# Performance work log

Measured on AMD Instinct MI355X. Metric: run time of the kernel, lower is better.

Reference implementation:

```python
import jax, jax.numpy as jnp
import numpy as np

TOP_K = 2
CAPACITY_FACTOR = 1.0


def setup_inputs() -> dict:
    key = jax.random.key(0)
    ks = jax.random.split(key, 4)
    S, M, E, V = 32768, 512, 64, 2048
    return {
        "x": jax.random.normal(ks[0], (S, M), jnp.float32),
        "wg": jax.random.normal(ks[1], (E, M), jnp.float32) * (1.0 / np.sqrt(M)),
        "fc1_w": jax.random.normal(ks[2], (E, M, V), jnp.float32) * (1.0 / np.sqrt(M)),
        "fc1_b": jnp.zeros((E, V), jnp.float32),
        "fc2_w": jax.random.normal(ks[3], (E, V, M), jnp.float32) * (1.0 / np.sqrt(V)),
        "fc2_b": jnp.zeros((E, M), jnp.float32),
    }


def _moe_forward(x, wg, fc1_w, fc1_b, fc2_w, fc2_b):
    S, M = x.shape
    E = wg.shape[0]
    K = TOP_K
    # capacity = top_k * int(cap_factor * ceil(S / E))  (static, from shapes)
    C = K * int(CAPACITY_FACTOR * ((S + E - 1) // E))

    # --- gating ---
    logits = x @ wg.T                                    # [S, E]
    gates = jax.nn.softmax(logits, axis=-1)              # [S, E]
    topk_idx = jax.lax.top_k(logits, K)[1]               # [S, K] int32
    masks = jax.nn.one_hot(topk_idx, E, dtype=logits.dtype)  # [S, K, E]
    gates_s = jnp.einsum('se,ske->sk', gates, masks)     # [S, K]

    # load-balance aux loss (fp32 path of load_balance)
    me = gates.sum(axis=0)                               # [E]
    ce = masks[:, 0, :].sum(axis=0)                      # [E]
    l_loss = jnp.sum(me * ce) * (E / (S * S))

    # --- cumsum capacity locations with per-k offsets (acc_base) ---
    counts = masks.sum(axis=0)                           # [K, E]
    prev_counts = jnp.concatenate(
        [jnp.zeros((1, E), logits.dtype), jnp.cumsum(counts, axis=0)[:-1]], axis=0)
    cums = jnp.cumsum(masks, axis=0) - 1.0               # fast_cumsum_sub_one per k
    locs = jnp.einsum('ske,ske->sk', cums + prev_counts[None], masks).astype(jnp.int32)

    # normalize top-k gates (top_k > 1 branch)
    denom = jnp.maximum(gates_s.sum(axis=1, keepdims=True),
                        jnp.finfo(gates_s.dtype).eps)
    gates_n = gates_s / denom                            # [S, K]

    # --- encode: scatter tokens into [E, C, M], overflow tokens dropped ---
    valid = locs < C                                     # [S, K]
    flat_pos = jnp.where(valid, topk_idx.astype(jnp.int32) * C + locs, E * C)
    src = jnp.broadcast_to(x[:, None, :], (S, K, M)).reshape(-1, M)
    disp = jnp.zeros((E * C + 1, M), x.dtype).at[flat_pos.reshape(-1)].add(src)
    disp = disp[:E * C].reshape(E, C, M)                 # world_size=1: AllToAll = id

    # --- fused FFN experts: relu(x @ fc1 + b1) @ fc2 + b2 ---
    h = jax.nn.relu(jnp.einsum('ecm,emv->ecv', disp, fc1_w) + fc1_b[:, None, :])
    eout = jnp.einsum('ecv,evm->ecm', h, fc2_w) + fc2_b[:, None, :]

    # --- decode/combine: gather expert slots, weight by normalized gates ---
    eflat = jnp.concatenate([eout.reshape(E * C, M),
                             jnp.zeros((1, M), eout.dtype)], axis=0)
    gathered = eflat[flat_pos]                           # [S, K, M]
    y = jnp.einsum('sk,skm->sm', gates_n * valid.astype(gates_n.dtype), gathered)
    return y, l_loss


def reference(x, wg, fc1_w, fc1_b, fc2_w, fc2_b):
    return _moe_forward(x, wg, fc1_w, fc1_b, fc2_w, fc2_b)
```

## Files before the change

### kernel.cpp

```cpp
#include <hip/hip_runtime.h>
#include <hip/hip_bf16.h>
#include <stdint.h>

#define S_TOK 32768
#define M_DIM 512
#define E_NUM 64
#define V_DIM 2048
#define CAP   1024

typedef __attribute__((ext_vector_type(8))) short short8;
typedef __attribute__((ext_vector_type(4))) float f32x4;

__device__ __forceinline__ unsigned short f2bf(float f) {
  unsigned int u = __float_as_uint(f);
  unsigned int r = (u + 0x7fffu + ((u >> 16) & 1u)) >> 16;
  return (unsigned short)r;
}
__device__ __forceinline__ float bf2f(unsigned short h) {
  return __uint_as_float(((unsigned int)h) << 16);
}

__device__ __forceinline__ void gload16(const void* g, void* lds) {
  __builtin_amdgcn_global_load_lds(
      (const __attribute__((address_space(1))) void*)g,
      (__attribute__((address_space(3))) void*)lds, 16, 0, 0);
}

#define GATE_BLKS (S_TOK / 16)
#define TR_BLKS   16384

struct PrepSmem {
  union {
    float ts[128][65];
    struct {
      float4 xs4[16 * 128];
      float mered[4][64];
      int cered[4][64];
    } g;
  };
};

__global__ __launch_bounds__(256) void prep_kernel(
    const float* __restrict__ x, const float* __restrict__ wg,
    int* __restrict__ topk, float* __restrict__ gates_n,
    float* __restrict__ me_part, int* __restrict__ ce_part,
    unsigned short* __restrict__ xbf,
    const float* __restrict__ w1, unsigned short* __restrict__ o1,
    const float* __restrict__ w2, unsigned short* __restrict__ o2) {
  __shared__ PrepSmem sm;
  int tid = threadIdx.x;

  if (blockIdx.x >= GATE_BLKS) {
    int t = blockIdx.x - GATE_BLKS;
    int which = t >> 13;
    t &= 8191;
    int R = which ? V_DIM : M_DIM;
    int Cc = which ? M_DIM : V_DIM;
    int nbx = Cc / 64;
    int b = t >> 7;
    int tt = t & 127;
    const float* ip = (which ? w2 : w1) + (size_t)b * R * Cc;
    unsigned short* op = (which ? o2 : o1) + (size_t)b * R * Cc;
    int c0 = (tt % nbx) * 64, r0 = (tt / nbx) * 128;
    #pragma unroll
    for (int i = 0; i < 8; ++i) {
      int chunk = i * 256 + tid;
      int row = chunk >> 4;
      int c4 = (chunk & 15) * 4;
      float4 v = *reinterpret_cast<const float4*>(&ip[(size_t)(r0 + row) * Cc + c0 + c4]);
      sm.ts[row][c4 + 0] = v.x; sm.ts[row][c4 + 1] = v.y;
      sm.ts[row][c4 + 2] = v.z; sm.ts[row][c4 + 3] = v.w;
    }
    __syncthreads();
    #pragma unroll
    for (int i = 0; i < 4; ++i) {
      int chunk = i * 256 + tid;
      int c = chunk >> 4;
      int m8 = (chunk & 15) * 8;
      short8 o;
      #pragma unroll
      for (int j = 0; j < 8; ++j) o[j] = (short)f2bf(sm.ts[m8 + j][c]);
      *reinterpret_cast<short8*>(&op[(size_t)(c0 + c) * R + r0 + m8]) = o;
    }
    return;
  }

  int l = tid & 63, w = tid >> 6;
  int tb = blockIdx.x * 16;
  const float4* xg4 = reinterpret_cast<const float4*>(x) + (size_t)tb * 128;
  ushort4* xb4 = reinterpret_cast<ushort4*>(xbf) + (size_t)tb * 128;
  #pragma unroll
  for (int i = 0; i < 8; ++i) {
    float4 v = xg4[i * 256 + tid];
    sm.g.xs4[i * 256 + tid] = v;
    ushort4 o;
    o.x = f2bf(v.x); o.y = f2bf(v.y); o.z = f2bf(v.z); o.w = f2bf(v.w);
    xb4[i * 256 + tid] = o;
  }
  __syncthreads();

  const float4* wg4 = reinterpret_cast<const float4*>(wg) + (size_t)l * 128;
  float acc[4] = {0.f, 0.f, 0.f, 0.f};
  for (int i0 = 0; i0 < 128; i0 += 8) {
    float4 wv[8];
    #pragma unroll
    for (int u = 0; u < 8; ++u) wv[u] = wg4[i0 + u];
    #pragma unroll
    for (int u = 0; u < 8; ++u) {
      #pragma unroll
      for (int t = 0; t < 4; ++t) {
        float4 xv = sm.g.xs4[(w * 4 + t) * 128 + i0 + u];
        acc[t] += xv.x * wv[u].x; acc[t] += xv.y * wv[u].y;
        acc[t] += xv.z * wv[u].z; acc[t] += xv.w * wv[u].w;
      }
    }
  }

  float melocal = 0.f;
  int celocal = 0;
  for (int t = 0; t < 4; ++t) {
    float v = acc[t];
    float bv = v; int bi = l;
    #pragma unroll
    for (int off = 32; off; off >>= 1) {
      float ov = __shfl_xor(bv, off);
      int oi = __shfl_xor(bi, off);
      if (ov > bv || (ov == bv && oi < bi)) { bv = ov; bi = oi; }
    }
    float v2 = (l == bi) ? -INFINITY : v;
    float bv2 = v2; int bi2 = l;
    #pragma unroll
    for (int off = 32; off; off >>= 1) {
      float ov = __shfl_xor(bv2, off);
      int oi = __shfl_xor(bi2, off);
      if (ov > bv2 || (ov == bv2 && oi < bi2)) { bv2 = ov; bi2 = oi; }
    }
    float ex = expf(v - bv);
    float s = ex;
    #pragma unroll
    for (int off = 32; off; off >>= 1) s += __shfl_xor(s, off);
    melocal += ex / s;
    if (l == bi) celocal += 1;
    if (l == 0) {
      int sidx = tb + w * 4 + t;
      topk[sidx * 2 + 0] = bi;
      topk[sidx * 2 + 1] = bi2;
      float g1 = 1.0f / s;
      float g2 = expf(bv2 - bv) / s;
      float denom = fmaxf(g1 + g2, 1.1920929e-07f);
      gates_n[sidx * 2 + 0] = g1 / denom;
      gates_n[sidx * 2 + 1] = g2 / denom;
    }
  }
  sm.g.mered[w][l] = melocal;
  sm.g.cered[w][l] = celocal;
  __syncthreads();
  if (tid < 64) {
    me_part[blockIdx.x * 64 + tid] =
        sm.g.mered[0][tid] + sm.g.mered[1][tid] + sm.g.mered[2][tid] + sm.g.mered[3][tid];
    ce_part[blockIdx.x * 64 + tid] =
        sm.g.cered[0][tid] + sm.g.cered[1][tid] + sm.g.cered[2][tid] + sm.g.cered[3][tid];
  }
}

__global__ __launch_bounds__(256) void rank_kernel(const int* __restrict__ topk,
                                                   int* __restrict__ dest,
                                                   int* __restrict__ slot_map) {
  int e = blockIdx.x;
  int tid = threadIdx.x;
  int l = tid & 63, w = tid >> 6;
  int4 minus1 = {-1, -1, -1, -1};
  reinterpret_cast<int4*>(slot_map + e * CAP)[tid] = minus1;

  const int2* tk = reinterpret_cast<const int2*>(topk);
  int base = tid * 128;
  int c0 = 0, c1 = 0;
  for (int j = 0; j < 128; ++j) {
    int2 p = tk[base + j];
    c0 += (p.x == e); c1 += (p.y == e);
  }
  int i0 = c0, i1 = c1;
  #pragma unroll
  for (int off = 1; off < 64; off <<= 1) {
    int t0 = __shfl_up(i0, off);
    int t1 = __shfl_up(i1, off);
    if (l >= off) { i0 += t0; i1 += t1; }
  }
  __shared__ int ws0[4], ws1[4], wo0[4], wo1[4], tot0s;
  if (l == 63) { ws0[w] = i0; ws1[w] = i1; }
  __syncthreads();
  if (tid == 0) {
    int a = 0, b = 0;
    #pragma unroll
    for (int j = 0; j < 4; ++j) { wo0[j] = a; a += ws0[j]; wo1[j] = b; b += ws1[j]; }
    tot0s = a;
  }
  __syncthreads();
  int loc0 = wo0[w] + i0 - c0;
  int loc1 = tot0s + wo1[w] + i1 - c1;
  for (int j = 0; j < 128; ++j) {
    int s = base + j;
    int2 p = tk[s];
    if (p.x == e) {
      int d = (loc0 < CAP) ? e * CAP + loc0 : -1;
      dest[s * 2] = d;
      if (d >= 0) slot_map[d] = s;
      loc0++;
    }
    if (p.y == e) {
      int d = (loc1 < CAP) ? e * CAP + loc1 : -1;
      dest[s * 2 + 1] = d;
      if (d >= 0) slot_map[d] = s;
      loc1++;
    }
  }
}

#define PH_TOP                                                                 \
  __builtin_amdgcn_sched_barrier(0);                                           \
  __builtin_amdgcn_s_barrier();                                                \
  asm volatile("s_waitcnt lgkmcnt(0)" ::: "memory");                           \
  __builtin_amdgcn_sched_barrier(0);                                           \
  __builtin_amdgcn_s_setprio(1);
#define PH_BOT                                                                 \
  __builtin_amdgcn_s_setprio(0);                                               \
  __builtin_amdgcn_sched_barrier(0);                                           \
  __builtin_amdgcn_s_barrier();

struct SmemGemm {
  union {
    struct {
      unsigned short A[2][256 * 64];
      unsigned short B[2][256 * 64];
    } st;
    unsigned short C[256 * 258];
  };
};

template <int KD, int ND, int NBX, int NBY, bool GATHER, bool RELU>
__global__ __launch_bounds__(512, 2) void gemm8_kernel(
    const unsigned short* __restrict__ A,
    const unsigned short* __restrict__ BT,
    const float* __restrict__ bias,
    const int* __restrict__ slot_map,
    unsigned short* __restrict__ out) {
  constexpr int NT = KD / 64;
  __shared__ SmemGemm sm;

  const int tid = threadIdx.x;
  const int l = tid & 63;
  const int w = tid >> 6;
  const int wm = w >> 2;
  const int wn = w & 3;
  const int lr = l & 15;
  const int lk8 = l >> 4;

  const int nwg = E_NUM * NBX * NBY;
  const int cpx = nwg >> 3;
  int lid = ((int)blockIdx.x % 8) * cpx + (int)blockIdx.x / 8;
  const int e = lid / (NBX * NBY);
  int rem = lid % (NBX * NBY);
  const int n0 = (rem / NBY) * 256;
  const int r0 = (rem % NBY) * 256;

  const int cg8 = (((l & 7) ^ (l >> 3)) * 8);

  uint32_t offA[2][2], offB[2][2], ldsA[2][2], ldsB[2][2];
  #pragma unroll
  for (int sel = 0; sel < 2; ++sel) {
    #pragma unroll
    for (int i = 0; i < 2; ++i) {
      int lr128 = i * 64 + w * 8 + (l >> 3);
      int ar = ((lr128 >> 6) * 128) + sel * 64 + (lr128 & 63);
      int br = ((lr128 >> 5) * 64) + sel * 32 + (lr128 & 31);
      ldsA[sel][i] = ar * 64 + (l & 7) * 8;
      ldsB[sel][i] = br * 64 + (l & 7) * 8;
      int arow;
      if (GATHER) {
        int s = slot_map[e * CAP + r0 + ar];
        if (s < 0) s = 0;
        arow = s;
      } else {
        arow = e * CAP + r0 + ar;
      }
      offA[sel][i] = (uint32_t)arow * KD + cg8;
      offB[sel][i] = (uint32_t)(n0 + br) * KD + cg8;
    }
  }
  const unsigned short* Bexp = BT + (size_t)e * ND * KD;

  const int sg0 = ((0 + lk8) ^ (lr & 7)) * 8;
  const int sg1 = ((4 + lk8) ^ (lr & 7)) * 8;

#define STAGE_A(sel, p, kt)                                                    \
  do {                                                                         \
    gload16(A + offA[sel][0] + (kt) * 64, &sm.st.A[p][ldsA[sel][0]]);          \
    gload16(A + offA[sel][1] + (kt) * 64, &sm.st.A[p][ldsA[sel][1]]);          \
  } while (0)
#define STAGE_B(sel, p, kt)                                                    \
  do {                                                                         \
    gload16(Bexp + offB[sel][0] + (kt) * 64, &sm.st.B[p][ldsB[sel][0]]);       \
    gload16(Bexp + offB[sel][1] + (kt) * 64, &sm.st.B[p][ldsB[sel][1]]);       \
  } while (0)
#define RD_A(p, mh, mi, ks)                                                    \
  (*reinterpret_cast<const short8*>(                                           \
      &sm.st.A[p][(wm * 128 + (mh) * 64 + (mi) * 16 + lr) * 64 + ((ks) ? sg1 : sg0)]))
#define RD_B(p, nh, ni, ks)                                                    \
  (*reinterpret_cast<const short8*>(                                           \
      &sm.st.B[p][(wn * 64 + (nh) * 32 + (ni) * 16 + lr) * 64 + ((ks) ? sg1 : sg0)]))

  short8 afr[2][4][2];
  short8 bfr[2][2];
  f32x4 acc[8][4];
  f32x4 zero = {0.f, 0.f, 0.f, 0.f};
  #pragma unroll
  for (int m = 0; m < 8; ++m)
    #pragma unroll
    for (int n = 0; n < 4; ++n) acc[m][n] = zero;

  STAGE_A(0, 0, 0); STAGE_A(1, 0, 0); STAGE_B(0, 0, 0); STAGE_B(1, 0, 0);
  STAGE_A(0, 1, 1); STAGE_A(1, 1, 1); STAGE_B(0, 1, 1);
  asm volatile("s_waitcnt vmcnt(6)" ::: "memory");
  __builtin_amdgcn_sched_barrier(0);
  __builtin_amdgcn_s_barrier();

#define GROUP(k, p)                                                            \
  {                                                                            \
               \
    _Pragma("unroll") for (int mi = 0; mi < 4; ++mi) {                         \
      afr[0][mi][0] = RD_A(p, 0, mi, 0);                                       \
      afr[0][mi][1] = RD_A(p, 0, mi, 1);                                       \
    }                                                                          \
    _Pragma("unroll") for (int ni = 0; ni < 2; ++ni) {                         \
      bfr[ni][0] = RD_B(p, 0, ni, 0);                                          \
      bfr[ni][1] = RD_B(p, 0, ni, 1);                                          \
    }                                                                          \
    if ((k) + 1 < NT) { STAGE_B(1, (p) ^ 1, (k) + 1); }                        \
    PH_TOP                                                                     \
    _Pragma("unroll") for (int mi = 0; mi < 4; ++mi)                           \
      _Pragma("unroll") for (int ni = 0; ni < 2; ++ni) {                       \
        acc[mi][ni] = __builtin_amdgcn_mfma_f32_16x16x32_bf16(                 \
            afr[0][mi][0], bfr[ni][0], acc[mi][ni], 0, 0, 0);                  \
        acc[mi][ni] = __builtin_amdgcn_mfma_f32_16x16x32_bf16(                 \
            afr[0][mi][1], bfr[ni][1], acc[mi][ni], 0, 0, 0);                  \
      }                                                                        \
    PH_BOT                                                                     \
                 \
    _Pragma("unroll") for (int mi = 0; mi < 4; ++mi) {                         \
      afr[1][mi][0] = RD_A(p, 1, mi, 0);                                       \
      afr[1][mi][1] = RD_A(p, 1, mi, 1);                                       \
    }                                                                          \
    if ((k) + 2 < NT) { STAGE_A(0, p, (k) + 2); }                              \
    PH_TOP                                                                     \
    _Pragma("unroll") for (int mi = 0; mi < 4; ++mi)                           \
      _Pragma("unroll") for (int ni = 0; ni < 2; ++ni) {                       \
        acc[4 + mi][ni] = __builtin_amdgcn_mfma_f32_16x16x32_bf16(             \
            afr[1][mi][0], bfr[ni][0], acc[4 + mi][ni], 0, 0, 0);              \
        acc[4 + mi][ni] = __builtin_amdgcn_mfma_f32_16x16x32_bf16(             \
            afr[1][mi][1], bfr[ni][1], acc[4 + mi][ni], 0, 0, 0);              \
      }                                                                        \
    PH_BOT                                                                     \
                 \
    _Pragma("unroll") for (int ni = 0; ni < 2; ++ni) {                         \
      bfr[ni][0] = RD_B(p, 1, ni, 0);                                          \
      bfr[ni][1] = RD_B(p, 1, ni, 1);                                          \
    }                                                                          \
    if ((k) + 2 < NT) { STAGE_A(1, p, (k) + 2); }                              \
    PH_TOP                                                                     \
    _Pragma("unroll") for (int mi = 0; mi < 4; ++mi)                           \
      _Pragma("unroll") for (int ni = 0; ni < 2; ++ni) {                       \
        acc[mi][2 + ni] = __builtin_amdgcn_mfma_f32_16x16x32_bf16(             \
            afr[0][mi][0], bfr[ni][0], acc[mi][2 + ni], 0, 0, 0);              \
        acc[mi][2 + ni] = __builtin_amdgcn_mfma_f32_16x16x32_bf16(             \
            afr[0][mi][1], bfr[ni][1], acc[mi][2 + ni], 0, 0, 0);              \
      }                                                                        \
    PH_BOT                                                                     \
             \
    if ((k) + 2 < NT) { STAGE_B(0, p, (k) + 2); }                              \
    __builtin_amdgcn_sched_barrier(0);                                         \
    __builtin_amdgcn_s_barrier();                                              \
    __builtin_amdgcn_s_setprio(1);                                             \
    _Pragma("unroll") for (int mi = 0; mi < 4; ++mi)                           \
      _Pragma("unroll") for (int ni = 0; ni < 2; ++ni) {                       \
        acc[4 + mi][2 + ni] = __builtin_amdgcn_mfma_f32_16x16x32_bf16(         \
            afr[1][mi][0], bfr[ni][0], acc[4 + mi][2 + ni], 0, 0, 0);          \
        acc[4 + mi][2 + ni] = __builtin_amdgcn_mfma_f32_16x16x32_bf16(         \
            afr[1][mi][1], bfr[ni][1], acc[4 + mi][2 + ni], 0, 0, 0);          \
      }                                                                        \
    __builtin_amdgcn_s_setprio(0);                                             \
    __builtin_amdgcn_sched_barrier(0);                                         \
    if ((k) + 2 < NT) {                                                        \
      asm volatile("s_waitcnt vmcnt(6)" ::: "memory");                         \
    } else {                                                                   \
      asm volatile("s_waitcnt vmcnt(0)" ::: "memory");                         \
    }                                                                          \
    __builtin_amdgcn_sched_barrier(0);                                         \
    __builtin_amdgcn_s_barrier();                                              \
  }

  for (int kk = 0; kk < NT / 2; ++kk) {
    int k0 = 2 * kk;
    GROUP(k0, 0)
    GROUP(k0 + 1, 1)
  }
#undef GROUP
#undef STAGE_A
#undef STAGE_B
#undef RD_A
#undef RD_B

  #pragma unroll
  for (int n = 0; n < 4; ++n) {
    int gcl = wn * 64 + n * 16 + lr;
    float bv = bias[e * ND + n0 + gcl];
    #pragma unroll
    for (int m = 0; m < 8; ++m) {
      int trow = wm * 128 + m * 16 + lk8 * 4;
      #pragma unroll
      for (int j = 0; j < 4; ++j) {
        float v = acc[m][n][j] + bv;
        if (RELU) v = fmaxf(v, 0.f);
        sm.C[(trow + j) * 258 + gcl] = f2bf(v);
      }
    }
  }
  __syncthreads();
  #pragma unroll
  for (int i = 0; i < 16; ++i) {
    int chunk = i * 512 + tid;
    int row = chunk >> 5;
    int c8 = chunk & 31;
    short8 v = *reinterpret_cast<const short8*>(&sm.C[row * 258 + c8 * 8]);
    *reinterpret_cast<short8*>(
        &out[((size_t)(e * CAP + r0 + row)) * ND + n0 + c8 * 8]) = v;
  }
}

__global__ __launch_bounds__(256) void decode_kernel(
    const unsigned short* __restrict__ Y, const int* __restrict__ dest,
    const float* __restrict__ gn, float* __restrict__ y,
    const float* __restrict__ me_part, const int* __restrict__ ce_part,
    float* __restrict__ loss_out) {
  int tid = threadIdx.x;
  if (blockIdx.x == gridDim.x - 1) {
    int e = tid & 63, ch = tid >> 6;
    float sme = 0.f, sce = 0.f;
    for (int j = 0; j < 512; ++j) {
      int idx = (ch * 512 + j) * 64 + e;
      sme += me_part[idx];
      sce += (float)ce_part[idx];
    }
    __shared__ float redm[4][64];
    __shared__ float redc[4][64];
    redm[ch][e] = sme;
    redc[ch][e] = sce;
    __syncthreads();
    if (tid < 64) {
      float m = redm[0][tid] + redm[1][tid] + redm[2][tid] + redm[3][tid];
      float c = redc[0][tid] + redc[1][tid] + redc[2][tid] + redc[3][tid];
      float p = m * c;
      #pragma unroll
      for (int off = 32; off; off >>= 1) p += __shfl_xor(p, off);
      if (tid == 0) loss_out[0] = p * ((float)E_NUM / ((float)S_TOK * (float)S_TOK));
    }
    return;
  }
  int t = blockIdx.x * 4 + (tid >> 6);
  int m0 = (tid & 63) * 8;
  int d0 = dest[t * 2 + 0], d1 = dest[t * 2 + 1];
  float g0 = gn[t * 2 + 0], g1 = gn[t * 2 + 1];
  float o[8];
  #pragma unroll
  for (int j = 0; j < 8; ++j) o[j] = 0.f;
  if (d0 >= 0) {
    short8 v = *reinterpret_cast<const short8*>(&Y[(size_t)d0 * M_DIM + m0]);
    #pragma unroll
    for (int j = 0; j < 8; ++j) o[j] += g0 * bf2f((unsigned short)v[j]);
  }
  if (d1 >= 0) {
    short8 v = *reinterpret_cast<const short8*>(&Y[(size_t)d1 * M_DIM + m0]);
    #pragma unroll
    for (int j = 0; j < 8; ++j) o[j] += g1 * bf2f((unsigned short)v[j]);
  }
  float4 o0 = {o[0], o[1], o[2], o[3]};
  float4 o1 = {o[4], o[5], o[6], o[7]};
  *reinterpret_cast<float4*>(&y[(size_t)t * M_DIM + m0]) = o0;
  *reinterpret_cast<float4*>(&y[(size_t)t * M_DIM + m0 + 4]) = o1;
}

extern "C" void kernel_launch(void* const* d_in, const int* in_sizes, int n_in,
                              void* d_out, int out_size, void* d_ws, size_t ws_size,
                              hipStream_t stream) {
  const float* x     = (const float*)d_in[0];
  const float* wg    = (const float*)d_in[1];
  const float* fc1_w = (const float*)d_in[2];
  const float* fc1_b = (const float*)d_in[3];
  const float* fc2_w = (const float*)d_in[4];
  const float* fc2_b = (const float*)d_in[5];
  float* y = (float*)d_out;
  float* loss_out = y + (size_t)S_TOK * M_DIM;

  char* ws = (char*)d_ws;
  size_t off = 0;
  auto alloc = [&](size_t bytes) {
    char* p = ws + off;
    off += (bytes + 255) & ~(size_t)255;
    return p;
  };
  unsigned short* wT1 = (unsigned short*)alloc((size_t)E_NUM * V_DIM * M_DIM * 2);
  unsigned short* wT2 = (unsigned short*)alloc((size_t)E_NUM * M_DIM * V_DIM * 2);
  unsigned short* H   = (unsigned short*)alloc((size_t)E_NUM * CAP * V_DIM * 2);
  unsigned short* xbf = (unsigned short*)alloc((size_t)S_TOK * M_DIM * 2);
  int*   topk     = (int*)alloc((size_t)S_TOK * 2 * 4);
  float* gatesn   = (float*)alloc((size_t)S_TOK * 2 * 4);
  int*   dest     = (int*)alloc((size_t)S_TOK * 2 * 4);
  int*   slot_map = (int*)alloc((size_t)E_NUM * CAP * 4);
  float* me_part  = (float*)alloc((size_t)GATE_BLKS * 64 * 4);
  int*   ce_part  = (int*)alloc((size_t)GATE_BLKS * 64 * 4);
  unsigned short* Y = wT1;

  prep_kernel<<<GATE_BLKS + TR_BLKS, 256, 0, stream>>>(
      x, wg, topk, gatesn, me_part, ce_part, xbf, fc1_w, wT1, fc2_w, wT2);

  rank_kernel<<<E_NUM, 256, 0, stream>>>(topk, dest, slot_map);

  gemm8_kernel<512, 2048, 8, 4, true, true>
      <<<E_NUM * 8 * 4, 512, 0, stream>>>(xbf, wT1, fc1_b, slot_map, H);
  gemm8_kernel<2048, 512, 2, 4, false, false>
      <<<E_NUM * 2 * 4, 512, 0, stream>>>(H, wT2, fc2_b, slot_map, Y);

  decode_kernel<<<S_TOK / 4 + 1, 256, 0, stream>>>(Y, dest, gatesn, y,
                                                   me_part, ce_part, loss_out);
}
```

Measured before the change: 767.3 us.

## Move fc2 weight transpose from prep kernel into fc1 GEMM epilogue

The fc2 weight fp32-to-bf16 transpose is taken out of the prep kernel and done at the tail of each fc1 GEMM block, with each of the 2048 blocks transposing eight 64x64 tiles. The aim is to shrink the memory-bound prep kernel and hide the transpose traffic behind fc1 GEMM work by sharing the machine with other blocks still computing. In exchange the fc1 GEMM blocks grow longer, use a smaller 64x64 tile, and add extra barriers.

```diff
diff --git a/kernel.cpp b/kernel.cpp
--- a/kernel.cpp
+++ b/kernel.cpp
@@ -27,7 +27,7 @@
 }
 
 #define GATE_BLKS (S_TOK / 16)
-#define TR_BLKS   16384
+#define TR1_BLKS  8192
 
 struct PrepSmem {
   union {
@@ -45,22 +45,18 @@
     int* __restrict__ topk, float* __restrict__ gates_n,
     float* __restrict__ me_part, int* __restrict__ ce_part,
     unsigned short* __restrict__ xbf,
-    const float* __restrict__ w1, unsigned short* __restrict__ o1,
-    const float* __restrict__ w2, unsigned short* __restrict__ o2) {
+    const float* __restrict__ w1, unsigned short* __restrict__ o1) {
   __shared__ PrepSmem sm;
   int tid = threadIdx.x;
 
   if (blockIdx.x >= GATE_BLKS) {
     int t = blockIdx.x - GATE_BLKS;
-    int which = t >> 13;
-    t &= 8191;
-    int R = which ? V_DIM : M_DIM;
-    int Cc = which ? M_DIM : V_DIM;
-    int nbx = Cc / 64;
     int b = t >> 7;
     int tt = t & 127;
-    const float* ip = (which ? w2 : w1) + (size_t)b * R * Cc;
-    unsigned short* op = (which ? o2 : o1) + (size_t)b * R * Cc;
+    const int R = M_DIM, Cc = V_DIM;
+    const int nbx = Cc / 64;
+    const float* ip = w1 + (size_t)b * R * Cc;
+    unsigned short* op = o1 + (size_t)b * R * Cc;
     int c0 = (tt % nbx) * 64, r0 = (tt / nbx) * 128;
     #pragma unroll
     for (int i = 0; i < 8; ++i) {
@@ -234,16 +230,19 @@
       unsigned short B[2][256 * 64];
     } st;
     unsigned short C[256 * 258];
+    float tsp[64][65];
   };
 };
 
-template <int KD, int ND, int NBX, int NBY, bool GATHER, bool RELU>
+template <int KD, int ND, int NBX, int NBY, bool GATHER, bool RELU, bool FC2T>
 __global__ __launch_bounds__(512, 2) void gemm8_kernel(
     const unsigned short* __restrict__ A,
     const unsigned short* __restrict__ BT,
     const float* __restrict__ bias,
     const int* __restrict__ slot_map,
-    unsigned short* __restrict__ out) {
+    unsigned short* __restrict__ out,
+    const float* __restrict__ w2,
+    unsigned short* __restrict__ o2) {
   constexpr int NT = KD / 64;
   __shared__ SmemGemm sm;
 
@@ -434,6 +433,39 @@
     *reinterpret_cast<short8*>(
         &out[((size_t)(e * CAP + r0 + row)) * ND + n0 + c8 * 8]) = v;
   }
+
+  if (FC2T) {
+    __syncthreads();
+    for (int tile = 0; tile < 8; ++tile) {
+      int g = (int)blockIdx.x * 8 + tile;
+      int b = g >> 8;
+      int tt = g & 255;
+      int tr0 = (tt >> 3) * 64;
+      int tc0 = (tt & 7) * 64;
+      const float* ip = w2 + (size_t)b * V_DIM * M_DIM;
+      unsigned short* op = o2 + (size_t)b * M_DIM * V_DIM;
+      #pragma unroll
+      for (int i2 = 0; i2 < 2; ++i2) {
+        int q = i2 * 512 + tid;
+        int row = q >> 4;
+        int c4 = (q & 15) * 4;
+        float4 v = *reinterpret_cast<const float4*>(
+            &ip[(size_t)(tr0 + row) * M_DIM + tc0 + c4]);
+        sm.tsp[row][c4 + 0] = v.x; sm.tsp[row][c4 + 1] = v.y;
+        sm.tsp[row][c4 + 2] = v.z; sm.tsp[row][c4 + 3] = v.w;
+      }
+      __syncthreads();
+      {
+        int c = tid >> 3;
+        int m8 = (tid & 7) * 8;
+        short8 o;
+        #pragma unroll
+        for (int j = 0; j < 8; ++j) o[j] = (short)f2bf(sm.tsp[m8 + j][c]);
+        *reinterpret_cast<short8*>(&op[(size_t)(tc0 + c) * V_DIM + tr0 + m8]) = o;
+      }
+      __syncthreads();
+    }
+  }
 }
 
 __global__ __launch_bounds__(256) void decode_kernel(
@@ -519,15 +551,15 @@
   int*   ce_part  = (int*)alloc((size_t)GATE_BLKS * 64 * 4);
   unsigned short* Y = wT1;
 
-  prep_kernel<<<GATE_BLKS + TR_BLKS, 256, 0, stream>>>(
-      x, wg, topk, gatesn, me_part, ce_part, xbf, fc1_w, wT1, fc2_w, wT2);
+  prep_kernel<<<GATE_BLKS + TR1_BLKS, 256, 0, stream>>>(
+      x, wg, topk, gatesn, me_part, ce_part, xbf, fc1_w, wT1);
 
   rank_kernel<<<E_NUM, 256, 0, stream>>>(topk, dest, slot_map);
 
-  gemm8_kernel<512, 2048, 8, 4, true, true>
-      <<<E_NUM * 8 * 4, 512, 0, stream>>>(xbf, wT1, fc1_b, slot_map, H);
-  gemm8_kernel<2048, 512, 2, 4, false, false>
-      <<<E_NUM * 2 * 4, 512, 0, stream>>>(H, wT2, fc2_b, slot_map, Y);
+  gemm8_kernel<512, 2048, 8, 4, true, true, true>
+      <<<E_NUM * 8 * 4, 512, 0, stream>>>(xbf, wT1, fc1_b, slot_map, H, fc2_w, wT2);
+  gemm8_kernel<2048, 512, 2, 4, false, false, false>
+      <<<E_NUM * 2 * 4, 512, 0, stream>>>(H, wT2, fc2_b, slot_map, Y, nullptr, nullptr);
 
   decode_kernel<<<S_TOK / 4 + 1, 256, 0, stream>>>(Y, dest, gatesn, y,
                                                    me_part, ce_part, loss_out);
```

Result: slower. 1.055 ms (+37.5%).
